# Performance work log

Hardware: AMD Instinct MI355X
Metric: run time of the kernel (lower is better)

The kernel has to match this reference:

```python
import jax, jax.numpy as jnp
import numpy as np

EMBED_DIM = 256
NUM_HEADS = 8
HEAD_DIM = EMBED_DIM // NUM_HEADS
SCALE = float(np.sqrt(HEAD_DIM))


def setup_inputs() -> dict:
    key = jax.random.key(0)
    ks = jax.random.split(key, 9)
    B, C, H, W = 4, EMBED_DIM, 48, 48
    s = 1.0 / np.sqrt(C)
    x = jax.random.normal(ks[0], (B, C, H, W), dtype=jnp.float32)
    # 1x1 convs == per-pixel channel matmuls; store as [out_c, in_c] weights + bias
    wq = jax.random.normal(ks[1], (C, C), dtype=jnp.float32) * s
    wk = jax.random.normal(ks[2], (C, C), dtype=jnp.float32) * s
    wv = jax.random.normal(ks[3], (C, C), dtype=jnp.float32) * s
    wo = jax.random.normal(ks[4], (C, C), dtype=jnp.float32) * s
    bq = jax.random.normal(ks[5], (C,), dtype=jnp.float32) * s
    bk = jax.random.normal(ks[6], (C,), dtype=jnp.float32) * s
    bv = jax.random.normal(ks[7], (C,), dtype=jnp.float32) * s
    bo = jax.random.normal(ks[8], (C,), dtype=jnp.float32) * s
    return {"x": x, "wq": wq, "bq": bq, "wk": wk, "bk": bk,
            "wv": wv, "bv": bv, "wo": wo, "bo": bo}


def reference(x, wq, bq, wk, bk, wv, bv, wo, bo):
    B, C, H, W = x.shape
    L = H * W
    xf = x.reshape(B, C, L)  # [B, C, L]
    def proj(w, b):
        y = jnp.einsum('oc,bcl->bol', w, xf) + b[None, :, None]
        return y.reshape(B, NUM_HEADS, HEAD_DIM, L)
    q = proj(wq, bq)  # [B, h, d, L]
    k = proj(wk, bk)
    v = proj(wv, bv)
    # scores: [B, h, Lq, Lk]
    attn = jnp.einsum('bhdq,bhdk->bhqk', q, k) / SCALE
    attn = jax.nn.softmax(attn, axis=-1)
    # dropout is identity in eval mode
    out = jnp.einsum('bhdk,bhqk->bhdq', v, attn)  # [B, h, d, L]
    out = out.reshape(B, C, L)
    out = jnp.einsum('oc,bcl->bol', wo, out) + bo[None, :, None]
    return out.reshape(B, C, H, W)
```

## Files before the change

kernel.cpp:

```cpp
#include <hip/hip_runtime.h>
#include <hip/hip_bf16.h>

typedef __attribute__((ext_vector_type(8))) short bf16x8;
typedef __attribute__((ext_vector_type(4))) float f32x4;
typedef __attribute__((ext_vector_type(16))) float f32x16;

#define DEV static __device__ __forceinline__

constexpr int Cc = 256;
constexpr int Ll = 2304;
constexpr float SM_C = 0.25503486f;

#if __has_builtin(__builtin_amdgcn_exp2f)
#define EXP2(x) __builtin_amdgcn_exp2f(x)
#else
#define EXP2(x) exp2f(x)
#endif
#if __has_builtin(__builtin_amdgcn_rcpf)
#define RCP(x) __builtin_amdgcn_rcpf(x)
#else
#define RCP(x) (1.0f / (x))
#endif

DEV unsigned short f2bf(float f) {
  union { float f; unsigned u; } v; v.f = f;
  unsigned r = v.u + 0x7FFFu + ((v.u >> 16) & 1u);
  return (unsigned short)(r >> 16);
}

DEV unsigned short f2bfc(float f) {
  union { __hip_bfloat16 h; unsigned short u; } c;
  c.h = __float2bfloat16(f);
  return c.u;
}

DEV unsigned packbf(float lo, float hi) {
  return (unsigned)f2bfc(lo) | ((unsigned)f2bfc(hi) << 16);
}

__global__ __launch_bounds__(256) void k_wconv(
    const float* __restrict__ wq, const float* __restrict__ wk,
    const float* __restrict__ wv, const float* __restrict__ wo,
    unsigned short* __restrict__ wb) {
  int m = blockIdx.y;
  const float* src = (m == 0) ? wq : (m == 1) ? wk : (m == 2) ? wv : wo;
  float sc = (m == 0) ? SM_C : 1.0f;
  int i = (blockIdx.x * 256 + threadIdx.x) * 8;
  float4 f0 = *(const float4*)&src[i];
  float4 f1 = *(const float4*)&src[i + 4];
  uint4 o;
  o.x = (unsigned)f2bf(f0.x * sc) | ((unsigned)f2bf(f0.y * sc) << 16);
  o.y = (unsigned)f2bf(f0.z * sc) | ((unsigned)f2bf(f0.w * sc) << 16);
  o.z = (unsigned)f2bf(f1.x * sc) | ((unsigned)f2bf(f1.y * sc) << 16);
  o.w = (unsigned)f2bf(f1.z * sc) | ((unsigned)f2bf(f1.w * sc) << 16);
  *(uint4*)&wb[(size_t)m * 65536 + i] = o;
}

__global__ __launch_bounds__(256) void k_xpose(const float* __restrict__ x,
                                               unsigned short* __restrict__ xt) {
  int b = blockIdx.z;
  int c0 = blockIdx.y * 32;
  int l = blockIdx.x * 256 + threadIdx.x;
  const float* xp = x + (size_t)b * Cc * Ll + l;
  unsigned short* op = xt + ((size_t)b * Ll + l) * Cc + c0;
  float v[32];
#pragma unroll
  for (int j = 0; j < 32; ++j) v[j] = xp[(size_t)(c0 + j) * Ll];
  unsigned u[16];
#pragma unroll
  for (int j = 0; j < 16; ++j)
    u[j] = (unsigned)f2bf(v[2 * j]) | ((unsigned)f2bf(v[2 * j + 1]) << 16);
  uint4* o4 = (uint4*)op;
#pragma unroll
  for (int j = 0; j < 4; ++j)
    o4[j] = make_uint4(u[4 * j], u[4 * j + 1], u[4 * j + 2], u[4 * j + 3]);
}

__global__ __launch_bounds__(256) void k_qkv(
    const unsigned short* __restrict__ xt, const unsigned short* __restrict__ wb,
    const float* __restrict__ bq, const float* __restrict__ bk,
    const float* __restrict__ bv,
    unsigned short* __restrict__ qt, unsigned short* __restrict__ kt,
    unsigned short* __restrict__ vm) {
  __shared__ __align__(16) unsigned short Bs[64][264];
  int b = blockIdx.z;
  int m0 = blockIdx.y * 64, n0 = blockIdx.x * 64;
  int tid = threadIdx.x, lane = tid & 63, wave = tid >> 6;
  int g = lane >> 4, cl = lane & 15;
  const uint4* bp = (const uint4*)(xt + ((size_t)b * Ll + n0) * 256);
#pragma unroll
  for (int j = 0; j < 8; ++j) {
    int idx = j * 256 + tid;
    *(uint4*)&Bs[idx >> 5][(idx & 31) * 8] = bp[idx];
  }
  __syncthreads();
  int ob = m0 + wave * 16 + g * 4;
  int h = ob >> 5, d0 = ob & 31;
#pragma unroll
  for (int p = 0; p < 3; ++p) {
    const unsigned short* Wrow =
        wb + (size_t)p * 65536 + (size_t)(m0 + wave * 16 + cl) * 256 + g * 8;
    bf16x8 af[8];
#pragma unroll
    for (int ks = 0; ks < 8; ++ks) af[ks] = *(const bf16x8*)&Wrow[ks * 32];
    f32x4 acc[4] = {};
#pragma unroll
    for (int ks = 0; ks < 8; ++ks) {
#pragma unroll
      for (int nf = 0; nf < 4; ++nf) {
        bf16x8 bb = *(const bf16x8*)&Bs[nf * 16 + cl][ks * 32 + g * 8];
        acc[nf] = __builtin_amdgcn_mfma_f32_16x16x32_bf16(af[ks], bb, acc[nf], 0, 0, 0);
      }
    }
    const float* bias = (p == 0) ? bq : (p == 1) ? bk : bv;
    float sc = (p == 0) ? SM_C : 1.0f;
    float b0 = bias[ob] * sc, b1 = bias[ob + 1] * sc;
    float b2 = bias[ob + 2] * sc, b3 = bias[ob + 3] * sc;
#pragma unroll
    for (int nf = 0; nf < 4; ++nf) {
      int l = n0 + nf * 16 + cl;
      float v0 = acc[nf][0] + b0, v1 = acc[nf][1] + b1;
      float v2 = acc[nf][2] + b2, v3 = acc[nf][3] + b3;
      if (p < 2) {
        unsigned short* dst = ((p == 0) ? qt : kt) +
            ((size_t)(b * 8 + h) * Ll + l) * 32 + d0;
        *(uint2*)dst = make_uint2(packbf(v0, v1), packbf(v2, v3));
      } else {
        size_t base = (size_t)(b * 8 + h) * 32 + d0;
        vm[(base + 0) * Ll + l] = f2bfc(v0);
        vm[(base + 1) * Ll + l] = f2bfc(v1);
        vm[(base + 2) * Ll + l] = f2bfc(v2);
        vm[(base + 3) * Ll + l] = f2bfc(v3);
      }
    }
  }
}

__global__ __launch_bounds__(256) void k_attn(
    const unsigned short* __restrict__ qt,
    const unsigned short* __restrict__ kt,
    const unsigned short* __restrict__ vm,
    unsigned short* __restrict__ aot) {
  __shared__ __align__(16) unsigned short Ks[2][64][36];
  __shared__ __align__(16) unsigned short Vs[2][32][68];
  __shared__ float Osh[2][32][33];
  __shared__ float Ssh[2][32];
  int bh = blockIdx.y, b = bh >> 3, h = bh & 7;
  int q0 = blockIdx.x * 64;
  int tid = threadIdx.x, wave = tid >> 6, lane = tid & 63;
  int qsub = wave >> 1, sstr = wave & 1;
  int hi = lane >> 5, c = lane & 31;

  const unsigned short* qb = qt + (size_t)bh * Ll * 32;
  const unsigned short* kb = kt + (size_t)bh * Ll * 32;
  const unsigned short* vb = vm + (size_t)bh * 32 * Ll;

  bf16x8 qf[2];
  qf[0] = *(const bf16x8*)&qb[(size_t)(q0 + qsub * 32 + c) * 32 + hi * 8];
  qf[1] = *(const bf16x8*)&qb[(size_t)(q0 + qsub * 32 + c) * 32 + 16 + hi * 8];

  bf16x8 ones;
#pragma unroll
  for (int i = 0; i < 8; ++i) ones[i] = (short)0x3F80;

  f32x16 oacc = {};
  f32x16 osum = {};

  int krow = tid >> 2, kcol = (tid & 3) * 8;
  int vrow = tid >> 3, vcol = (tid & 7) * 8;

  {
    uint4 k0 = *(const uint4*)&kb[(size_t)krow * 32 + kcol];
    uint4 k1 = *(const uint4*)&kb[(size_t)(64 + krow) * 32 + kcol];
    uint4 v0 = *(const uint4*)&vb[(size_t)vrow * Ll + vcol];
    uint4 v1 = *(const uint4*)&vb[(size_t)vrow * Ll + 64 + vcol];
    *(uint2*)&Ks[0][krow][kcol] = make_uint2(k0.x, k0.y);
    *(uint2*)&Ks[0][krow][kcol + 4] = make_uint2(k0.z, k0.w);
    *(uint2*)&Ks[1][krow][kcol] = make_uint2(k1.x, k1.y);
    *(uint2*)&Ks[1][krow][kcol + 4] = make_uint2(k1.z, k1.w);
    *(uint2*)&Vs[0][vrow][vcol] = make_uint2(v0.x, v0.y);
    *(uint2*)&Vs[0][vrow][vcol + 4] = make_uint2(v0.z, v0.w);
    *(uint2*)&Vs[1][vrow][vcol] = make_uint2(v1.x, v1.y);
    *(uint2*)&Vs[1][vrow][vcol + 4] = make_uint2(v1.z, v1.w);
  }

  uint4 kr0, kr1, vr0, vr1;
  for (int j = 0; j < 18; ++j) {
    __syncthreads();
    if (j < 17) {
      int ta = (2 * j + 2) * 64, tb = ta + 64;
      kr0 = *(const uint4*)&kb[(size_t)(ta + krow) * 32 + kcol];
      kr1 = *(const uint4*)&kb[(size_t)(tb + krow) * 32 + kcol];
      vr0 = *(const uint4*)&vb[(size_t)vrow * Ll + ta + vcol];
      vr1 = *(const uint4*)&vb[(size_t)vrow * Ll + tb + vcol];
    }
    f32x16 p_[2];
#pragma unroll
    for (int fb = 0; fb < 2; ++fb) {
      f32x16 z = {};
#pragma unroll
      for (int dh = 0; dh < 2; ++dh) {
        union { bf16x8 v; uint2 u2[2]; } kf;
        kf.u2[0] = *(const uint2*)&Ks[sstr][fb * 32 + c][dh * 16 + hi * 8];
        kf.u2[1] = *(const uint2*)&Ks[sstr][fb * 32 + c][dh * 16 + hi * 8 + 4];
        z = __builtin_amdgcn_mfma_f32_32x32x16_bf16(kf.v, qf[dh], z, 0, 0, 0);
      }
      p_[fb] = z;
    }
#pragma unroll
    for (int fb = 0; fb < 2; ++fb)
#pragma unroll
      for (int r = 0; r < 16; ++r) p_[fb][r] = EXP2(p_[fb][r]);
    union { unsigned w[16]; bf16x8 v8[4]; } Wp;
#pragma unroll
    for (int m = 0; m < 16; ++m)
      Wp.w[m] = packbf(p_[m >> 3][2 * (m & 7)], p_[m >> 3][2 * (m & 7) + 1]);
#pragma unroll
    for (int ks = 0; ks < 4; ++ks) {
      union { bf16x8 v; uint2 u2[2]; } vf;
      vf.u2[0] = *(const uint2*)&Vs[sstr][c][ks * 16 + hi * 4];
      vf.u2[1] = *(const uint2*)&Vs[sstr][c][ks * 16 + 8 + hi * 4];
      oacc = __builtin_amdgcn_mfma_f32_32x32x16_bf16(Wp.v8[ks], vf.v, oacc, 0, 0, 0);
      osum = __builtin_amdgcn_mfma_f32_32x32x16_bf16(Wp.v8[ks], ones, osum, 0, 0, 0);
    }
    __syncthreads();
    if (j < 17) {
      *(uint2*)&Ks[0][krow][kcol] = make_uint2(kr0.x, kr0.y);
      *(uint2*)&Ks[0][krow][kcol + 4] = make_uint2(kr0.z, kr0.w);
      *(uint2*)&Ks[1][krow][kcol] = make_uint2(kr1.x, kr1.y);
      *(uint2*)&Ks[1][krow][kcol + 4] = make_uint2(kr1.z, kr1.w);
      *(uint2*)&Vs[0][vrow][vcol] = make_uint2(vr0.x, vr0.y);
      *(uint2*)&Vs[0][vrow][vcol + 4] = make_uint2(vr0.z, vr0.w);
      *(uint2*)&Vs[1][vrow][vcol] = make_uint2(vr1.x, vr1.y);
      *(uint2*)&Vs[1][vrow][vcol + 4] = make_uint2(vr1.z, vr1.w);
    }
  }

  if (sstr == 1) {
#pragma unroll
    for (int r = 0; r < 16; ++r) {
      int qrl = (r & 3) + 8 * (r >> 2) + 4 * hi;
      Osh[qsub][qrl][c] = oacc[r];
      if (c == 0) Ssh[qsub][qrl] = osum[r];
    }
  }
  __syncthreads();
  if (sstr == 0) {
#pragma unroll
    for (int r = 0; r < 16; ++r) {
      int qrl = (r & 3) + 8 * (r >> 2) + 4 * hi;
      float ot = oacc[r] + Osh[qsub][qrl][c];
      float st = osum[r] + Ssh[qsub][qrl];
      float val = ot * RCP(st);
      aot[((size_t)b * Ll + q0 + qsub * 32 + qrl) * 256 + h * 32 + c] = f2bfc(val);
    }
  }
}

__global__ __launch_bounds__(256) void k_oproj(
    const unsigned short* __restrict__ aot, const unsigned short* __restrict__ wb,
    const float* __restrict__ bo, float* __restrict__ out) {
  __shared__ __align__(16) unsigned short Bs[64][264];
  int b = blockIdx.z;
  int m0 = blockIdx.y * 64, n0 = blockIdx.x * 64;
  int tid = threadIdx.x, lane = tid & 63, wave = tid >> 6;
  int g = lane >> 4, cl = lane & 15;
  const uint4* bp = (const uint4*)(aot + ((size_t)b * Ll + n0) * 256);
#pragma unroll
  for (int j = 0; j < 8; ++j) {
    int idx = j * 256 + tid;
    *(uint4*)&Bs[idx >> 5][(idx & 31) * 8] = bp[idx];
  }
  __syncthreads();
  const unsigned short* Wrow =
      wb + (size_t)3 * 65536 + (size_t)(m0 + wave * 16 + cl) * 256 + g * 8;
  bf16x8 af[8];
#pragma unroll
  for (int ks = 0; ks < 8; ++ks) af[ks] = *(const bf16x8*)&Wrow[ks * 32];
  f32x4 acc[4] = {};
#pragma unroll
  for (int ks = 0; ks < 8; ++ks) {
#pragma unroll
    for (int nf = 0; nf < 4; ++nf) {
      bf16x8 bb = *(const bf16x8*)&Bs[nf * 16 + cl][ks * 32 + g * 8];
      acc[nf] = __builtin_amdgcn_mfma_f32_16x16x32_bf16(af[ks], bb, acc[nf], 0, 0, 0);
    }
  }
  int ob = m0 + wave * 16 + g * 4;
  float b0 = bo[ob], b1 = bo[ob + 1], b2 = bo[ob + 2], b3 = bo[ob + 3];
#pragma unroll
  for (int nf = 0; nf < 4; ++nf) {
    int l = n0 + nf * 16 + cl;
    float* dst = out + ((size_t)b * 256 + ob) * Ll + l;
    dst[(size_t)0 * Ll] = acc[nf][0] + b0;
    dst[(size_t)1 * Ll] = acc[nf][1] + b1;
    dst[(size_t)2 * Ll] = acc[nf][2] + b2;
    dst[(size_t)3 * Ll] = acc[nf][3] + b3;
  }
}

extern "C" void kernel_launch(void* const* d_in, const int* in_sizes, int n_in,
                              void* d_out, int out_size, void* d_ws, size_t ws_size,
                              hipStream_t stream) {
  (void)in_sizes; (void)n_in; (void)out_size; (void)ws_size;
  const float* x  = (const float*)d_in[0];
  const float* wq = (const float*)d_in[1];
  const float* bq = (const float*)d_in[2];
  const float* wk = (const float*)d_in[3];
  const float* bk = (const float*)d_in[4];
  const float* wv = (const float*)d_in[5];
  const float* bv = (const float*)d_in[6];
  const float* wo = (const float*)d_in[7];
  const float* bo = (const float*)d_in[8];
  float* out = (float*)d_out;

  const size_t CH = (size_t)4 * Ll * Cc;
  unsigned short* xt = (unsigned short*)d_ws;
  unsigned short* qt = xt + CH;
  unsigned short* kt = xt + 2 * CH;
  unsigned short* vm = xt + 3 * CH;
  unsigned short* wbq = xt + 4 * CH;
  unsigned short* aot = xt;

  k_wconv<<<dim3(32, 4), 256, 0, stream>>>(wq, wk, wv, wo, wbq);
  k_xpose<<<dim3(9, 8, 4), 256, 0, stream>>>(x, xt);
  k_qkv<<<dim3(36, 4, 4), 256, 0, stream>>>(xt, wbq, bq, bk, bv, qt, kt, vm);
  k_attn<<<dim3(36, 32), 256, 0, stream>>>(qt, kt, vm, aot);
  k_oproj<<<dim3(36, 4, 4), 256, 0, stream>>>(aot, wbq, bo, out);
}
```

Measured before the change: 153.3 us.

## Rewrite attention as single-wave blocks loading K/V directly into registers

```diff
diff --git a/kernel.cpp b/kernel.cpp
--- a/kernel.cpp
+++ b/kernel.cpp
@@ -126,134 +126,97 @@
             ((size_t)(b * 8 + h) * Ll + l) * 32 + d0;
         *(uint2*)dst = make_uint2(packbf(v0, v1), packbf(v2, v3));
       } else {
+        int lp = n0 + nf * 16 + ((cl & 3) | ((cl & 4) << 1) | ((cl & 8) >> 1));
         size_t base = (size_t)(b * 8 + h) * 32 + d0;
-        vm[(base + 0) * Ll + l] = f2bfc(v0);
-        vm[(base + 1) * Ll + l] = f2bfc(v1);
-        vm[(base + 2) * Ll + l] = f2bfc(v2);
-        vm[(base + 3) * Ll + l] = f2bfc(v3);
+        vm[(base + 0) * Ll + lp] = f2bfc(v0);
+        vm[(base + 1) * Ll + lp] = f2bfc(v1);
+        vm[(base + 2) * Ll + lp] = f2bfc(v2);
+        vm[(base + 3) * Ll + lp] = f2bfc(v3);
       }
     }
   }
 }
 
-__global__ __launch_bounds__(256) void k_attn(
+DEV void attn_step(uint4 k0, uint4 k1, uint4 k2, uint4 k3,
+                   uint4 v0, uint4 v1, uint4 v2, uint4 v3,
+                   bf16x8 qf0, bf16x8 qf1, bf16x8 ones,
+                   f32x16& oacc, f32x16& osum) {
+  union U { uint4 u; bf16x8 v; };
+  U a0{k0}, a1{k1}, a2{k2}, a3{k3}, w0{v0}, w1{v1}, w2{v2}, w3{v3};
+  f32x16 p0 = {}, p1 = {};
+  p0 = __builtin_amdgcn_mfma_f32_32x32x16_bf16(a0.v, qf0, p0, 0, 0, 0);
+  p0 = __builtin_amdgcn_mfma_f32_32x32x16_bf16(a1.v, qf1, p0, 0, 0, 0);
+  p1 = __builtin_amdgcn_mfma_f32_32x32x16_bf16(a2.v, qf0, p1, 0, 0, 0);
+  p1 = __builtin_amdgcn_mfma_f32_32x32x16_bf16(a3.v, qf1, p1, 0, 0, 0);
+#pragma unroll
+  for (int r = 0; r < 16; ++r) { p0[r] = EXP2(p0[r]); p1[r] = EXP2(p1[r]); }
+  union { unsigned w[16]; bf16x8 v8[4]; } Wp;
+#pragma unroll
+  for (int m = 0; m < 8; ++m) {
+    Wp.w[m] = packbf(p0[2 * m], p0[2 * m + 1]);
+    Wp.w[8 + m] = packbf(p1[2 * m], p1[2 * m + 1]);
+  }
+  oacc = __builtin_amdgcn_mfma_f32_32x32x16_bf16(Wp.v8[0], w0.v, oacc, 0, 0, 0);
+  osum = __builtin_amdgcn_mfma_f32_32x32x16_bf16(Wp.v8[0], ones, osum, 0, 0, 0);
+  oacc = __builtin_amdgcn_mfma_f32_32x32x16_bf16(Wp.v8[1], w1.v, oacc, 0, 0, 0);
+  osum = __builtin_amdgcn_mfma_f32_32x32x16_bf16(Wp.v8[1], ones, osum, 0, 0, 0);
+  oacc = __builtin_amdgcn_mfma_f32_32x32x16_bf16(Wp.v8[2], w2.v, oacc, 0, 0, 0);
+  osum = __builtin_amdgcn_mfma_f32_32x32x16_bf16(Wp.v8[2], ones, osum, 0, 0, 0);
+  oacc = __builtin_amdgcn_mfma_f32_32x32x16_bf16(Wp.v8[3], w3.v, oacc, 0, 0, 0);
+  osum = __builtin_amdgcn_mfma_f32_32x32x16_bf16(Wp.v8[3], ones, osum, 0, 0, 0);
+}
+
+#define LDK(d0, d1, d2, d3, J)                              \
+  d0 = *(const uint4*)(kl0 + ((J) * 64 + 0) * 32 + 0);      \
+  d1 = *(const uint4*)(kl0 + ((J) * 64 + 0) * 32 + 16);     \
+  d2 = *(const uint4*)(kl0 + ((J) * 64 + 32) * 32 + 0);     \
+  d3 = *(const uint4*)(kl0 + ((J) * 64 + 32) * 32 + 16);
+#define LDV(d0, d1, d2, d3, J)                  \
+  d0 = *(const uint4*)(vl0 + (J) * 64 + 0);     \
+  d1 = *(const uint4*)(vl0 + (J) * 64 + 16);    \
+  d2 = *(const uint4*)(vl0 + (J) * 64 + 32);    \
+  d3 = *(const uint4*)(vl0 + (J) * 64 + 48);
+
+__global__ __launch_bounds__(64, 3) void k_attn(
     const unsigned short* __restrict__ qt,
     const unsigned short* __restrict__ kt,
-    const unsigned short* __restrict__ vm,
+    const unsigned short* __restrict__ vp,
     unsigned short* __restrict__ aot) {
-  __shared__ __align__(16) unsigned short Ks[2][64][36];
-  __shared__ __align__(16) unsigned short Vs[2][32][68];
-  __shared__ float Osh[2][32][33];
-  __shared__ float Ssh[2][32];
-  int bh = blockIdx.y, b = bh >> 3, h = bh & 7;
-  int q0 = blockIdx.x * 64;
-  int tid = threadIdx.x, wave = tid >> 6, lane = tid & 63;
-  int qsub = wave >> 1, sstr = wave & 1;
+  int n = blockIdx.x;
+  int bh = n & 31, qw = n >> 5;
+  int b = bh >> 3, h = bh & 7;
+  int lane = threadIdx.x;
   int hi = lane >> 5, c = lane & 31;
 
   const unsigned short* qb = qt + (size_t)bh * Ll * 32;
-  const unsigned short* kb = kt + (size_t)bh * Ll * 32;
-  const unsigned short* vb = vm + (size_t)bh * 32 * Ll;
-
-  bf16x8 qf[2];
-  qf[0] = *(const bf16x8*)&qb[(size_t)(q0 + qsub * 32 + c) * 32 + hi * 8];
-  qf[1] = *(const bf16x8*)&qb[(size_t)(q0 + qsub * 32 + c) * 32 + 16 + hi * 8];
+  const unsigned short* kl0 = kt + (size_t)bh * Ll * 32 + (size_t)c * 32 + hi * 8;
+  const unsigned short* vl0 = vp + (size_t)bh * 32 * Ll + (size_t)c * Ll + hi * 8;
+
+  bf16x8 qf0 = *(const bf16x8*)&qb[(size_t)(qw * 32 + c) * 32 + hi * 8];
+  bf16x8 qf1 = *(const bf16x8*)&qb[(size_t)(qw * 32 + c) * 32 + 16 + hi * 8];
 
   bf16x8 ones;
 #pragma unroll
   for (int i = 0; i < 8; ++i) ones[i] = (short)0x3F80;
 
-  f32x16 oacc = {};
-  f32x16 osum = {};
-
-  int krow = tid >> 2, kcol = (tid & 3) * 8;
-  int vrow = tid >> 3, vcol = (tid & 7) * 8;
-
-  {
-    uint4 k0 = *(const uint4*)&kb[(size_t)krow * 32 + kcol];
-    uint4 k1 = *(const uint4*)&kb[(size_t)(64 + krow) * 32 + kcol];
-    uint4 v0 = *(const uint4*)&vb[(size_t)vrow * Ll + vcol];
-    uint4 v1 = *(const uint4*)&vb[(size_t)vrow * Ll + 64 + vcol];
-    *(uint2*)&Ks[0][krow][kcol] = make_uint2(k0.x, k0.y);
-    *(uint2*)&Ks[0][krow][kcol + 4] = make_uint2(k0.z, k0.w);
-    *(uint2*)&Ks[1][krow][kcol] = make_uint2(k1.x, k1.y);
-    *(uint2*)&Ks[1][krow][kcol + 4] = make_uint2(k1.z, k1.w);
-    *(uint2*)&Vs[0][vrow][vcol] = make_uint2(v0.x, v0.y);
-    *(uint2*)&Vs[0][vrow][vcol + 4] = make_uint2(v0.z, v0.w);
-    *(uint2*)&Vs[1][vrow][vcol] = make_uint2(v1.x, v1.y);
-    *(uint2*)&Vs[1][vrow][vcol + 4] = make_uint2(v1.z, v1.w);
-  }
-
-  uint4 kr0, kr1, vr0, vr1;
-  for (int j = 0; j < 18; ++j) {
-    __syncthreads();
-    if (j < 17) {
-      int ta = (2 * j + 2) * 64, tb = ta + 64;
-      kr0 = *(const uint4*)&kb[(size_t)(ta + krow) * 32 + kcol];
-      kr1 = *(const uint4*)&kb[(size_t)(tb + krow) * 32 + kcol];
-      vr0 = *(const uint4*)&vb[(size_t)vrow * Ll + ta + vcol];
-      vr1 = *(const uint4*)&vb[(size_t)vrow * Ll + tb + vcol];
-    }
-    f32x16 p_[2];
-#pragma unroll
-    for (int fb = 0; fb < 2; ++fb) {
-      f32x16 z = {};
-#pragma unroll
-      for (int dh = 0; dh < 2; ++dh) {
-        union { bf16x8 v; uint2 u2[2]; } kf;
-        kf.u2[0] = *(const uint2*)&Ks[sstr][fb * 32 + c][dh * 16 + hi * 8];
-        kf.u2[1] = *(const uint2*)&Ks[sstr][fb * 32 + c][dh * 16 + hi * 8 + 4];
-        z = __builtin_amdgcn_mfma_f32_32x32x16_bf16(kf.v, qf[dh], z, 0, 0, 0);
-      }
-      p_[fb] = z;
-    }
-#pragma unroll
-    for (int fb = 0; fb < 2; ++fb)
-#pragma unroll
-      for (int r = 0; r < 16; ++r) p_[fb][r] = EXP2(p_[fb][r]);
-    union { unsigned w[16]; bf16x8 v8[4]; } Wp;
-#pragma unroll
-    for (int m = 0; m < 16; ++m)
-      Wp.w[m] = packbf(p_[m >> 3][2 * (m & 7)], p_[m >> 3][2 * (m & 7) + 1]);
-#pragma unroll
-    for (int ks = 0; ks < 4; ++ks) {
-      union { bf16x8 v; uint2 u2[2]; } vf;
-      vf.u2[0] = *(const uint2*)&Vs[sstr][c][ks * 16 + hi * 4];
-      vf.u2[1] = *(const uint2*)&Vs[sstr][c][ks * 16 + 8 + hi * 4];
-      oacc = __builtin_amdgcn_mfma_f32_32x32x16_bf16(Wp.v8[ks], vf.v, oacc, 0, 0, 0);
-      osum = __builtin_amdgcn_mfma_f32_32x32x16_bf16(Wp.v8[ks], ones, osum, 0, 0, 0);
-    }
-    __syncthreads();
-    if (j < 17) {
-      *(uint2*)&Ks[0][krow][kcol] = make_uint2(kr0.x, kr0.y);
-      *(uint2*)&Ks[0][krow][kcol + 4] = make_uint2(kr0.z, kr0.w);
-      *(uint2*)&Ks[1][krow][kcol] = make_uint2(kr1.x, kr1.y);
-      *(uint2*)&Ks[1][krow][kcol + 4] = make_uint2(kr1.z, kr1.w);
-      *(uint2*)&Vs[0][vrow][vcol] = make_uint2(vr0.x, vr0.y);
-      *(uint2*)&Vs[0][vrow][vcol + 4] = make_uint2(vr0.z, vr0.w);
-      *(uint2*)&Vs[1][vrow][vcol] = make_uint2(vr1.x, vr1.y);
-      *(uint2*)&Vs[1][vrow][vcol + 4] = make_uint2(vr1.z, vr1.w);
-    }
-  }
-
-  if (sstr == 1) {
-#pragma unroll
-    for (int r = 0; r < 16; ++r) {
-      int qrl = (r & 3) + 8 * (r >> 2) + 4 * hi;
-      Osh[qsub][qrl][c] = oacc[r];
-      if (c == 0) Ssh[qsub][qrl] = osum[r];
-    }
-  }
-  __syncthreads();
-  if (sstr == 0) {
-#pragma unroll
-    for (int r = 0; r < 16; ++r) {
-      int qrl = (r & 3) + 8 * (r >> 2) + 4 * hi;
-      float ot = oacc[r] + Osh[qsub][qrl][c];
-      float st = osum[r] + Ssh[qsub][qrl];
-      float val = ot * RCP(st);
-      aot[((size_t)b * Ll + q0 + qsub * 32 + qrl) * 256 + h * 32 + c] = f2bfc(val);
-    }
+  f32x16 oacc = {}, osum = {};
+
+  uint4 ka0, ka1, ka2, ka3, kb0, kb1, kb2, kb3, va0, va1, va2, va3;
+  LDK(ka0, ka1, ka2, ka3, 0);
+  for (int j = 0; j < 36; j += 2) {
+    LDV(va0, va1, va2, va3, j);
+    LDK(kb0, kb1, kb2, kb3, j + 1);
+    attn_step(ka0, ka1, ka2, ka3, va0, va1, va2, va3, qf0, qf1, ones, oacc, osum);
+    LDV(va0, va1, va2, va3, j + 1);
+    if (j + 2 < 36) { LDK(ka0, ka1, ka2, ka3, j + 2); }
+    attn_step(kb0, kb1, kb2, kb3, va0, va1, va2, va3, qf0, qf1, ones, oacc, osum);
+  }
+
+  unsigned short* ob = aot + ((size_t)b * Ll + (size_t)qw * 32) * 256 + h * 32 + c;
+#pragma unroll
+  for (int r = 0; r < 16; ++r) {
+    int qrl = (r & 3) + 8 * (r >> 2) + 4 * hi;
+    ob[(size_t)qrl * 256] = f2bfc(oacc[r] * RCP(osum[r]));
   }
 }
 
@@ -325,6 +288,6 @@
   k_wconv<<<dim3(32, 4), 256, 0, stream>>>(wq, wk, wv, wo, wbq);
   k_xpose<<<dim3(9, 8, 4), 256, 0, stream>>>(x, xt);
   k_qkv<<<dim3(36, 4, 4), 256, 0, stream>>>(xt, wbq, bq, bk, bv, qt, kt, vm);
-  k_attn<<<dim3(36, 32), 256, 0, stream>>>(qt, kt, vm, aot);
+  k_attn<<<dim3(2304), 64, 0, stream>>>(qt, kt, vm, aot);
   k_oproj<<<dim3(36, 4, 4), 256, 0, stream>>>(aot, wbq, bo, out);
 }
```

Result: slower. 164.0 us (+7.0%).
